# Kernel optimization log

Hardware: AMD Instinct MI355X
Metric: run time of the kernel (lower is better)

The kernel has to match this reference:

```python
import jax, jax.numpy as jnp
import numpy as np

B, T, J, D = 32, 1024, 256, 512

def setup_inputs() -> dict:
    key = jax.random.key(0)
    k1, k2, k3 = jax.random.split(key, 3)
    h = jax.random.normal(k1, (B, T, D), dtype=jnp.float32)
    u = jax.random.normal(k2, (B, J, D), dtype=jnp.float32)
    w = jax.random.normal(k3, (1, 3 * D), dtype=jnp.float32) * 0.05
    return {"h": h, "u": u, "w": w}

def reference(h, u, w):
    # S[b,i,j] = w . concat([h_i, u_j, h_i*u_j])
    # Algebraic decomposition: w = [w_h, w_u, w_m]
    d = h.shape[-1]
    w = w[0]
    w_h, w_u, w_m = w[:d], w[d:2*d], w[2*d:]
    # [B,T,1] + [B,1,J] + [B,T,J]
    term_h = jnp.einsum('btd,d->bt', h, w_h)[:, :, None]
    term_u = jnp.einsum('bjd,d->bj', u, w_u)[:, None, :]
    term_m = jnp.einsum('btd,bjd->btj', h * w_m, u)
    return term_h + term_u + term_m
```

## Files before the change

kernel.cpp:

```cpp
#include <hip/hip_runtime.h>
#include <hip/hip_bf16.h>
#include <stdint.h>

#define B_ 32
#define T_ 1024
#define J_ 256
#define D_ 512

typedef __attribute__((ext_vector_type(8))) short short8;
typedef __attribute__((ext_vector_type(4))) float floatx4;

__global__ __launch_bounds__(256) void prep_u_kernel(
    const float* __restrict__ u, const float* __restrict__ w,
    __hip_bfloat16* __restrict__ B2, float* __restrict__ tu)
{
    int row  = blockIdx.x * 4 + (threadIdx.x >> 6);
    int lane = threadIdx.x & 63;
    const float* src = u + (size_t)row * D_;
    int base = lane * 8;

    float4 v0  = *(const float4*)(src + base);
    float4 v1  = *(const float4*)(src + base + 4);
    float4 wh0 = *(const float4*)(w + base);
    float4 wh1 = *(const float4*)(w + base + 4);
    float4 wu0 = *(const float4*)(w + D_ + base);
    float4 wu1 = *(const float4*)(w + D_ + base + 4);
    float4 wm0 = *(const float4*)(w + 2*D_ + base);
    float4 wm1 = *(const float4*)(w + 2*D_ + base + 4);

    float s = v0.x*wu0.x + v0.y*wu0.y + v0.z*wu0.z + v0.w*wu0.w
            + v1.x*wu1.x + v1.y*wu1.y + v1.z*wu1.z + v1.w*wu1.w;

    float vals[8] = {
        v0.x*wm0.x + wh0.x, v0.y*wm0.y + wh0.y,
        v0.z*wm0.z + wh0.z, v0.w*wm0.w + wh0.w,
        v1.x*wm1.x + wh1.x, v1.y*wm1.y + wh1.y,
        v1.z*wm1.z + wh1.z, v1.w*wm1.w + wh1.w };

    union { __hip_bfloat16 b[8]; uint4 q; } pk;
#pragma unroll
    for (int i = 0; i < 8; i++) pk.b[i] = __float2bfloat16(vals[i]);
    *(uint4*)(B2 + (size_t)row * D_ + base) = pk.q;

#pragma unroll
    for (int off = 32; off > 0; off >>= 1) s += __shfl_down(s, off, 64);
    if (lane == 0) tu[row] = s;
}

__device__ inline void gload_lds16(const void* g, void* l) {
    __builtin_amdgcn_global_load_lds(
        (__attribute__((address_space(1))) void*)(g),
        (__attribute__((address_space(3))) void*)(l),
        16, 0, 0);
}

__global__ __launch_bounds__(512, 4) void gemm_kernel(
    const float* __restrict__ h,
    const __hip_bfloat16* __restrict__ B2,
    const float* __restrict__ tu,
    float* __restrict__ out)
{
    __shared__ __align__(16) __hip_bfloat16 sB[128 * 256];

    const int b   = blockIdx.y;
    const int tM  = blockIdx.x >> 1;
    const int tN  = blockIdx.x & 1;
    const int tid = threadIdx.x;
    const int w = tid >> 6, lane = tid & 63;

    const int fr = lane & 15;
    const int kq = lane >> 4;

    const float* Aw = h + ((size_t)b * T_ + tM * 128 + w * 16 + fr) * D_;
    const __hip_bfloat16* Bb = B2 + ((size_t)b * J_ + tN * 128) * D_;

    floatx4 acc[8];
#pragma unroll
    for (int n = 0; n < 8; n++) acc[n] = (floatx4)0.0f;

    for (int p = 0; p < 2; p++) {
#pragma unroll
        for (int i = 0; i < 8; i++) {
            int q  = i * 512 + tid;
            int j  = q >> 5;
            int c  = (q & 31) ^ (j & 31);
            gload_lds16(Bb + (size_t)j * D_ + p * 256 + c * 8, sB + q * 8);
        }
        __syncthreads();

#pragma unroll
        for (int ks = 0; ks < 8; ks++) {
            const float* ap = Aw + p * 256 + ks * 32 + kq * 8;
            float4 a0 = *(const float4*)(ap);
            float4 a1 = *(const float4*)(ap + 4);
            union { __hip_bfloat16 e[8]; short8 v; } af;
            af.e[0]=__float2bfloat16(a0.x); af.e[1]=__float2bfloat16(a0.y);
            af.e[2]=__float2bfloat16(a0.z); af.e[3]=__float2bfloat16(a0.w);
            af.e[4]=__float2bfloat16(a1.x); af.e[5]=__float2bfloat16(a1.y);
            af.e[6]=__float2bfloat16(a1.z); af.e[7]=__float2bfloat16(a1.w);
#pragma unroll
            for (int n = 0; n < 8; n++) {
                int j = n * 16 + fr;
                int c = ks * 4 + kq;
                short8 bf = *(const short8*)(sB + ((j * 32) + (c ^ (j & 31))) * 8);
                acc[n] = __builtin_amdgcn_mfma_f32_16x16x32_bf16(
                    af.v, bf, acc[n], 0, 0, 0);
            }
        }
        __syncthreads();
    }

    const size_t outB = (size_t)b * T_ * J_;
    const int r0 = tM * 128 + w * 16 + (lane >> 4) * 4;
    const float* tub = tu + b * J_;
#pragma unroll
    for (int n = 0; n < 8; n++) {
        int col = tN * 128 + n * 16 + fr;
        float tuv = tub[col];
#pragma unroll
        for (int r = 0; r < 4; r++) {
            out[outB + (size_t)(r0 + r) * J_ + col] = acc[n][r] + tuv;
        }
    }
}

extern "C" void kernel_launch(void* const* d_in, const int* in_sizes, int n_in,
                              void* d_out, int out_size, void* d_ws, size_t ws_size,
                              hipStream_t stream)
{
    const float* h = (const float*)d_in[0];
    const float* u = (const float*)d_in[1];
    const float* w = (const float*)d_in[2];
    float* out = (float*)d_out;

    uint8_t* ws = (uint8_t*)d_ws;
    __hip_bfloat16* B2 = (__hip_bfloat16*)ws;
    float* tu = (float*)(ws + (size_t)B_ * J_ * D_ * 2);

    prep_u_kernel<<<dim3(B_ * J_ / 4), 256, 0, stream>>>(u, w, B2, tu);

    gemm_kernel<<<dim3((T_ / 128) * (J_ / 128), B_), 512, 0, stream>>>(h, B2, tu, out);
}
```

Measured before the change: 131.7 us.

## Widen GEMM tile to full J with 1024 threads and double-buffered LDS

Each block now covers all 256 J columns for its 128 rows, using 16 waves arranged as 8 row groups by 2 column groups. Each h row is therefore read and converted only once instead of twice. The B operand is streamed in four K-chunks of 128 through two LDS buffers, so the load of the next chunk overlaps the MFMA work on the current one. In exchange, LDS use grows to 128KB per block and the grid shrinks to 256 blocks, which limits each CU to one block and reduces latency hiding.

Result: no change. 129.6 us (-1.6%).

```diff
diff --git a/kernel.cpp b/kernel.cpp
--- a/kernel.cpp
+++ b/kernel.cpp
@@ -54,43 +54,55 @@
         16, 0, 0);
 }
 
-__global__ __launch_bounds__(512, 4) void gemm_kernel(
+__global__ __launch_bounds__(1024, 4) void gemm_kernel(
     const float* __restrict__ h,
     const __hip_bfloat16* __restrict__ B2,
     const float* __restrict__ tu,
     float* __restrict__ out)
 {
-    __shared__ __align__(16) __hip_bfloat16 sB[128 * 256];
+    __shared__ __align__(16) __hip_bfloat16 sB[2][256 * 128];
 
     const int b   = blockIdx.y;
-    const int tM  = blockIdx.x >> 1;
-    const int tN  = blockIdx.x & 1;
+    const int tM  = blockIdx.x;
     const int tid = threadIdx.x;
     const int w = tid >> 6, lane = tid & 63;
+    const int wr = w >> 1, wc = w & 1;
 
     const int fr = lane & 15;
     const int kq = lane >> 4;
 
-    const float* Aw = h + ((size_t)b * T_ + tM * 128 + w * 16 + fr) * D_;
-    const __hip_bfloat16* Bb = B2 + ((size_t)b * J_ + tN * 128) * D_;
+    const float* Aw = h + ((size_t)b * T_ + tM * 128 + wr * 16 + fr) * D_;
+    const __hip_bfloat16* Bb = B2 + (size_t)b * J_ * D_;
 
     floatx4 acc[8];
 #pragma unroll
     for (int n = 0; n < 8; n++) acc[n] = (floatx4)0.0f;
 
-    for (int p = 0; p < 2; p++) {
 #pragma unroll
-        for (int i = 0; i < 8; i++) {
-            int q  = i * 512 + tid;
-            int j  = q >> 5;
-            int c  = (q & 31) ^ (j & 31);
-            gload_lds16(Bb + (size_t)j * D_ + p * 256 + c * 8, sB + q * 8);
+    for (int i = 0; i < 4; i++) {
+        int q = i * 1024 + tid;
+        int j = q >> 4;
+        int c = (q & 15) ^ (j & 15);
+        gload_lds16(Bb + (size_t)j * D_ + c * 8, &sB[0][q * 8]);
+    }
+    __syncthreads();
+
+    for (int p = 0; p < 4; p++) {
+        if (p < 3) {
+#pragma unroll
+            for (int i = 0; i < 4; i++) {
+                int q = i * 1024 + tid;
+                int j = q >> 4;
+                int c = (q & 15) ^ (j & 15);
+                gload_lds16(Bb + (size_t)j * D_ + (p + 1) * 128 + c * 8,
+                            &sB[(p + 1) & 1][q * 8]);
+            }
         }
-        __syncthreads();
+        const __hip_bfloat16* sBp = sB[p & 1];
 
 #pragma unroll
-        for (int ks = 0; ks < 8; ks++) {
-            const float* ap = Aw + p * 256 + ks * 32 + kq * 8;
+        for (int ks = 0; ks < 4; ks++) {
+            const float* ap = Aw + p * 128 + ks * 32 + kq * 8;
             float4 a0 = *(const float4*)(ap);
             float4 a1 = *(const float4*)(ap + 4);
             union { __hip_bfloat16 e[8]; short8 v; } af;
@@ -100,9 +112,9 @@
             af.e[6]=__float2bfloat16(a1.z); af.e[7]=__float2bfloat16(a1.w);
 #pragma unroll
             for (int n = 0; n < 8; n++) {
-                int j = n * 16 + fr;
+                int j = wc * 128 + n * 16 + fr;
                 int c = ks * 4 + kq;
-                short8 bf = *(const short8*)(sB + ((j * 32) + (c ^ (j & 31))) * 8);
+                short8 bf = *(const short8*)(sBp + (j * 16 + (c ^ (j & 15))) * 8);
                 acc[n] = __builtin_amdgcn_mfma_f32_16x16x32_bf16(
                     af.v, bf, acc[n], 0, 0, 0);
             }
@@ -111,11 +123,11 @@
     }
 
     const size_t outB = (size_t)b * T_ * J_;
-    const int r0 = tM * 128 + w * 16 + (lane >> 4) * 4;
+    const int r0 = tM * 128 + wr * 16 + (lane >> 4) * 4;
     const float* tub = tu + b * J_;
 #pragma unroll
     for (int n = 0; n < 8; n++) {
-        int col = tN * 128 + n * 16 + fr;
+        int col = wc * 128 + n * 16 + fr;
         float tuv = tub[col];
 #pragma unroll
         for (int r = 0; r < 4; r++) {
@@ -139,5 +151,5 @@
 
     prep_u_kernel<<<dim3(B_ * J_ / 4), 256, 0, stream>>>(u, w, B2, tu);
 
-    gemm_kernel<<<dim3((T_ / 128) * (J_ / 128), B_), 512, 0, stream>>>(h, B2, tu, out);
+    gemm_kernel<<<dim3(T_ / 128, B_), 1024, 0, stream>>>(h, B2, tu, out);
 }
```

## Pre-swizzle B into MFMA fragment layout and load directly from global, dropping LDS

Applied to the files above, without the earlier changes.

The prep kernel now writes the bf16 u-operand in an MFMA-fragment-ordered layout, so each lane of the GEMM can load its B fragment with one contiguous 16-byte global load. The GEMM drops the LDS staging, its barriers and the XOR swizzle. It uses 256 threads per block, with each wave computing two 16-row M tiles so that every B fragment is reused twice. Loads for the next k-step are register double-buffered. In exchange, every wave re-reads B from global or L2 memory instead of sharing it through LDS, and register pressure rises.

Measured after the change: 142.4 us. 8.1% more time.

```diff
diff --git a/kernel.cpp b/kernel.cpp
--- a/kernel.cpp
+++ b/kernel.cpp
@@ -12,7 +12,7 @@
 
 __global__ __launch_bounds__(256) void prep_u_kernel(
     const float* __restrict__ u, const float* __restrict__ w,
-    __hip_bfloat16* __restrict__ B2, float* __restrict__ tu)
+    __hip_bfloat16* __restrict__ B2f, float* __restrict__ tu)
 {
     int row  = blockIdx.x * 4 + (threadIdx.x >> 6);
     int lane = threadIdx.x & 63;
@@ -40,86 +40,106 @@
     union { __hip_bfloat16 b[8]; uint4 q; } pk;
 #pragma unroll
     for (int i = 0; i < 8; i++) pk.b[i] = __float2bfloat16(vals[i]);
-    *(uint4*)(B2 + (size_t)row * D_ + base) = pk.q;
+
+    int b  = row >> 8;
+    int j  = row & 255;
+    int n  = j >> 4, fr = j & 15;
+    int ks = lane >> 2, kq = lane & 3;
+    size_t dst = ((((size_t)b * 16 + n) * 16 + ks) * 512) + (kq * 16 + fr) * 8;
+    *(uint4*)(B2f + dst) = pk.q;
 
 #pragma unroll
     for (int off = 32; off > 0; off >>= 1) s += __shfl_down(s, off, 64);
     if (lane == 0) tu[row] = s;
 }
 
-__device__ inline void gload_lds16(const void* g, void* l) {
-    __builtin_amdgcn_global_load_lds(
-        (__attribute__((address_space(1))) void*)(g),
-        (__attribute__((address_space(3))) void*)(l),
-        16, 0, 0);
-}
-
-__global__ __launch_bounds__(512, 4) void gemm_kernel(
+__global__ __launch_bounds__(256, 2) void gemm_kernel(
     const float* __restrict__ h,
-    const __hip_bfloat16* __restrict__ B2,
+    const __hip_bfloat16* __restrict__ B2f,
     const float* __restrict__ tu,
     float* __restrict__ out)
 {
-    __shared__ __align__(16) __hip_bfloat16 sB[128 * 256];
-
     const int b   = blockIdx.y;
     const int tM  = blockIdx.x >> 1;
     const int tN  = blockIdx.x & 1;
     const int tid = threadIdx.x;
     const int w = tid >> 6, lane = tid & 63;
-
     const int fr = lane & 15;
     const int kq = lane >> 4;
 
-    const float* Aw = h + ((size_t)b * T_ + tM * 128 + w * 16 + fr) * D_;
-    const __hip_bfloat16* Bb = B2 + ((size_t)b * J_ + tN * 128) * D_;
+    const float* A0 = h + ((size_t)b * T_ + tM * 128 + w * 32 + fr) * D_ + kq * 8;
+    const float* A1 = A0 + 16 * D_;
+    const __hip_bfloat16* Bf =
+        B2f + (((size_t)b * 16 + tN * 8) * 16) * 512 + lane * 8;
 
-    floatx4 acc[8];
+    floatx4 acc[2][8];
 #pragma unroll
-    for (int n = 0; n < 8; n++) acc[n] = (floatx4)0.0f;
+    for (int mi = 0; mi < 2; mi++)
+#pragma unroll
+        for (int n = 0; n < 8; n++) acc[mi][n] = (floatx4)0.0f;
 
-    for (int p = 0; p < 2; p++) {
-#pragma unroll
-        for (int i = 0; i < 8; i++) {
-            int q  = i * 512 + tid;
-            int j  = q >> 5;
-            int c  = (q & 31) ^ (j & 31);
-            gload_lds16(Bb + (size_t)j * D_ + p * 256 + c * 8, sB + q * 8);
-        }
-        __syncthreads();
+    short8 bC[8], bN[8];
+    float4 aC[2][2], aN[2][2];
 
 #pragma unroll
-        for (int ks = 0; ks < 8; ks++) {
-            const float* ap = Aw + p * 256 + ks * 32 + kq * 8;
-            float4 a0 = *(const float4*)(ap);
-            float4 a1 = *(const float4*)(ap + 4);
-            union { __hip_bfloat16 e[8]; short8 v; } af;
-            af.e[0]=__float2bfloat16(a0.x); af.e[1]=__float2bfloat16(a0.y);
-            af.e[2]=__float2bfloat16(a0.z); af.e[3]=__float2bfloat16(a0.w);
-            af.e[4]=__float2bfloat16(a1.x); af.e[5]=__float2bfloat16(a1.y);
-            af.e[6]=__float2bfloat16(a1.z); af.e[7]=__float2bfloat16(a1.w);
+    for (int n = 0; n < 8; n++)
+        bC[n] = *(const short8*)(Bf + (n * 16 + 0) * 512);
+    aC[0][0] = *(const float4*)(A0);      aC[0][1] = *(const float4*)(A0 + 4);
+    aC[1][0] = *(const float4*)(A1);      aC[1][1] = *(const float4*)(A1 + 4);
+
 #pragma unroll
-            for (int n = 0; n < 8; n++) {
-                int j = n * 16 + fr;
-                int c = ks * 4 + kq;
-                short8 bf = *(const short8*)(sB + ((j * 32) + (c ^ (j & 31))) * 8);
-                acc[n] = __builtin_amdgcn_mfma_f32_16x16x32_bf16(
-                    af.v, bf, acc[n], 0, 0, 0);
+    for (int ks = 0; ks < 16; ks++) {
+        if (ks < 15) {
+#pragma unroll
+            for (int n = 0; n < 8; n++)
+                bN[n] = *(const short8*)(Bf + (n * 16 + ks + 1) * 512);
+            const float* p0 = A0 + (ks + 1) * 32;
+            const float* p1 = A1 + (ks + 1) * 32;
+            aN[0][0] = *(const float4*)(p0); aN[0][1] = *(const float4*)(p0 + 4);
+            aN[1][0] = *(const float4*)(p1); aN[1][1] = *(const float4*)(p1 + 4);
+        }
+
+        short8 af[2];
+#pragma unroll
+        for (int mi = 0; mi < 2; mi++) {
+            union { __hip_bfloat16 e[8]; short8 v; } pk;
+            pk.e[0]=__float2bfloat16(aC[mi][0].x); pk.e[1]=__float2bfloat16(aC[mi][0].y);
+            pk.e[2]=__float2bfloat16(aC[mi][0].z); pk.e[3]=__float2bfloat16(aC[mi][0].w);
+            pk.e[4]=__float2bfloat16(aC[mi][1].x); pk.e[5]=__float2bfloat16(aC[mi][1].y);
+            pk.e[6]=__float2bfloat16(aC[mi][1].z); pk.e[7]=__float2bfloat16(aC[mi][1].w);
+            af[mi] = pk.v;
+        }
+
+#pragma unroll
+        for (int mi = 0; mi < 2; mi++)
+#pragma unroll
+            for (int n = 0; n < 8; n++)
+                acc[mi][n] = __builtin_amdgcn_mfma_f32_16x16x32_bf16(
+                    af[mi], bC[n], acc[mi][n], 0, 0, 0);
+
+        if (ks < 15) {
+#pragma unroll
+            for (int n = 0; n < 8; n++) bC[n] = bN[n];
+#pragma unroll
+            for (int mi = 0; mi < 2; mi++) {
+                aC[mi][0] = aN[mi][0]; aC[mi][1] = aN[mi][1];
             }
         }
-        __syncthreads();
     }
 
     const size_t outB = (size_t)b * T_ * J_;
-    const int r0 = tM * 128 + w * 16 + (lane >> 4) * 4;
     const float* tub = tu + b * J_;
 #pragma unroll
-    for (int n = 0; n < 8; n++) {
-        int col = tN * 128 + n * 16 + fr;
-        float tuv = tub[col];
+    for (int mi = 0; mi < 2; mi++) {
+        int r0 = tM * 128 + w * 32 + mi * 16 + kq * 4;
 #pragma unroll
-        for (int r = 0; r < 4; r++) {
-            out[outB + (size_t)(r0 + r) * J_ + col] = acc[n][r] + tuv;
+        for (int n = 0; n < 8; n++) {
+            int col = tN * 128 + n * 16 + fr;
+            float tuv = tub[col];
+#pragma unroll
+            for (int r = 0; r < 4; r++) {
+                out[outB + (size_t)(r0 + r) * J_ + col] = acc[mi][n][r] + tuv;
+            }
         }
     }
 }
@@ -134,10 +154,10 @@
     float* out = (float*)d_out;
 
     uint8_t* ws = (uint8_t*)d_ws;
-    __hip_bfloat16* B2 = (__hip_bfloat16*)ws;
+    __hip_bfloat16* B2f = (__hip_bfloat16*)ws;
     float* tu = (float*)(ws + (size_t)B_ * J_ * D_ * 2);
 
-    prep_u_kernel<<<dim3(B_ * J_ / 4), 256, 0, stream>>>(u, w, B2, tu);
+    prep_u_kernel<<<dim3(B_ * J_ / 4), 256, 0, stream>>>(u, w, B2f, tu);
 
-    gemm_kernel<<<dim3((T_ / 128) * (J_ / 128), B_), 512, 0, stream>>>(h, B2, tu, out);
+    gemm_kernel<<<dim3((T_ / 128) * (J_ / 128), B_), 256, 0, stream>>>(h, B2f, tu, out);
 }
```
